# Kernel tuning notes

Hardware: AMD Instinct MI355X
Metric: run time of the kernel (lower is better)

The kernel has to match this reference:

```python
import jax, jax.numpy as jnp
import numpy as np

# module hyperparams (match init_kwargs)
C, K, S, RATIO, GC = 64, 7, 2, 2, 16
G = C // GC                      # 4 groups
KK = K * K                       # 49
NS = int(RATIO * S)              # 4
NN = NS * NS                     # 16
PAD = (K - 1) // 2               # 3
C1_IN = G * (2 * K * GC + KK)    # 1092
C1_OUT = G * NN * KK // 10       # 313
C2_OUT = G * NN * KK             # 3136
EPS = 1e-5


def _unfold(x, k, s, p):
    # torch.nn.Unfold: patches ordered (C, ki, kj) channel-major
    B, Cc, H, W = x.shape
    xp = jnp.pad(x, ((0, 0), (0, 0), (p, p), (p, p)))
    Ho = (H + 2 * p - k) // s + 1
    Wo = (W + 2 * p - k) // s + 1
    rows = jnp.arange(Ho)[:, None] * s + jnp.arange(k)[None, :]      # (Ho,k)
    cols = jnp.arange(Wo)[:, None] * s + jnp.arange(k)[None, :]      # (Wo,k)
    pat = xp[:, :, rows[:, :, None, None], cols[None, None, :, :]]   # (B,C,Ho,k,Wo,k)
    return pat.transpose(0, 1, 3, 5, 2, 4)                            # (B,C,k,k,Ho,Wo)


def setup_inputs() -> dict:
    key = jax.random.key(0)
    ks = jax.random.split(key, 5)
    x = jax.random.normal(ks[0], (8, C, 64, 64), dtype=jnp.float32)
    w1 = jax.random.normal(ks[1], (C1_OUT, C1_IN), dtype=jnp.float32) * 0.02
    gamma = jnp.ones((C1_OUT,), dtype=jnp.float32)   # BN weight (constant_init 1)
    beta = jnp.zeros((C1_OUT,), dtype=jnp.float32)   # BN bias
    w2 = jax.random.normal(ks[2], (C2_OUT, C1_OUT), dtype=jnp.float32) * 0.02
    b2 = jnp.zeros((C2_OUT,), dtype=jnp.float32)
    return {"x": x, "w1": w1, "gamma": gamma, "beta": beta, "w2": w2, "b2": b2}


def reference(x, w1, gamma, beta, w2, b2):
    B, _, H, W = x.shape
    pat = _unfold(x, K, S, PAD)                          # (B,C,K,K,Ho,Wo)
    Ho, Wo = pat.shape[-2], pat.shape[-1]
    xg = pat.reshape(B, G, GC, K, K, Ho, Wo)
    # three axis-wise max pools -> per-pixel descriptor
    x1 = xg.max(axis=2).reshape(B, G * K * K, Ho, Wo)
    x2 = xg.max(axis=3).reshape(B, G * GC * K, Ho, Wo)
    x3 = xg.max(axis=4).reshape(B, G * GC * K, Ho, Wo)
    feat = jnp.concatenate([x1, x2, x3], axis=1)         # (B, C1_IN, Ho, Wo)
    # conv1: 1x1 conv (no bias) + BN (batch stats) + ReLU
    h = jnp.einsum('bchw,oc->bohw', feat, w1)
    mu = h.mean(axis=(0, 2, 3), keepdims=True)
    var = h.var(axis=(0, 2, 3), keepdims=True)
    h = gamma[None, :, None, None] * (h - mu) * jax.lax.rsqrt(var + EPS) + beta[None, :, None, None]
    h = jax.nn.relu(h)
    # conv2: 1x1 conv with bias
    h2 = jnp.einsum('bchw,oc->bohw', h, w2) + b2[None, :, None, None]
    wt = h2.reshape(B, G, KK, NN, Ho, Wo)
    wt = jax.nn.softmax(wt, axis=2)                      # softmax over kernel positions
    # softmax-weighted patch reduction (mean over k*k)
    xk = xg.reshape(B, G, GC, KK, Ho, Wo)
    out = jnp.einsum('bgckhw,bgknhw->bgcnhw', xk, wt) / KK
    out = out.reshape(B, C, NS, NS, Ho, Wo)
    out = out.transpose(0, 1, 4, 2, 5, 3).reshape(B, C, Ho * NS, Wo * NS)
    return out
```

## Files before the change

kernel.cpp:

```cpp
#include <hip/hip_runtime.h>

namespace {
constexpr int kB    = 8;
constexpr int kC    = 64;
constexpr int kH    = 64, kW = 64;
constexpr int kNP   = 8192;
constexpr int kC1In = 1092;
constexpr int kKP   = 1152;
constexpr int kC1Out= 313;
constexpr int kC2Out= 3136;
constexpr int kC1P  = 320;
constexpr int kRowS = 56;
constexpr int kPosS = 16 * kRowS + 8;
}

typedef __attribute__((ext_vector_type(8))) short bf16x8;
typedef __attribute__((ext_vector_type(8))) _Float16 f16x8;
typedef __attribute__((ext_vector_type(2))) _Float16 h16x2;
typedef __attribute__((ext_vector_type(4))) float f32x4;

__device__ __forceinline__ unsigned short f2bf(float f) {
    unsigned u = __float_as_uint(f);
    unsigned r = (u + 0x7fffu + ((u >> 16) & 1u)) >> 16;
    return (unsigned short)r;
}

__global__ void k_w2split(const float* __restrict__ w2, bf16x8* __restrict__ w2t) {
    int idx = blockIdx.x * 256 + threadIdx.x;
    int lane = idx & 63;
    int t = (idx >> 6) % 10;
    int k = (idx / 640) % 49;
    int g = idx / 31360;
    int n = lane & 15, c0 = t * 32 + ((lane >> 4) << 3);
    int row = g * 784 + k * 16 + n;
    bf16x8 hi;
    #pragma unroll
    for (int e = 0; e < 8; ++e) {
        int c = c0 + e;
        float v = (c < kC1Out) ? w2[(size_t)row * kC1Out + c] : 0.f;
        hi[e] = (short)f2bf(v);
    }
    w2t[idx] = hi;
}

__global__ void k_w1cvt(const float* __restrict__ w1, unsigned short* __restrict__ w1s,
                        float* __restrict__ stats) {
    int idx = blockIdx.x * 256 + threadIdx.x;
    if (idx < 640) stats[idx] = 0.f;
    if (idx >= kC1P * kKP) return;
    int r = idx / kKP, c = idx - r * kKP;
    float v = (r < kC1Out && c < kC1In) ? w1[(size_t)r * kC1In + c] : 0.f;
    w1s[idx] = f2bf(v);
}

__global__ __launch_bounds__(256) void k_feat(const float* __restrict__ x,
                                              unsigned short* __restrict__ feat_bf) {
    __shared__ float xs[16 * 7 * 40];
    int tid = threadIdx.x;
    int g = blockIdx.x, pt = blockIdx.y;
    int p0 = pt * 16;
    int b = p0 >> 10, i = (p0 >> 5) & 31, j0 = p0 & 31;
    int y0 = 2 * i - 3, xbase = 2 * j0 - 3;
    const float* xb = x + ((size_t)(b * 64 + g * 16) << 12);

    for (int idx = tid; idx < 16 * 7 * 40; idx += 256) {
        int ch = idx / 280, r2 = idx - ch * 280;
        int row = r2 / 40, col = r2 - row * 40;
        int yy = y0 + row, xx = xbase + col;
        float v = 0.f;
        if ((unsigned)yy < 64u && (unsigned)xx < 64u)
            v = xb[(ch << 12) + (yy << 6) + xx];
        xs[idx] = v;
    }
    __syncthreads();

    for (int o = tid; o < 16 * 273; o += 256) {
        int pos = o / 273, c = o - pos * 273;
        float m = -INFINITY;
        int cg;
        if (c < 49) {
            int a = c / 7, bk = c - a * 7;
            int base = a * 40 + 2 * pos + bk;
            #pragma unroll
            for (int ch = 0; ch < 16; ++ch) m = fmaxf(m, xs[ch * 280 + base]);
            cg = g * 49 + c;
        } else if (c < 161) {
            int r = c - 49;
            int ch = r / 7, bk = r - ch * 7;
            int base = ch * 280 + 2 * pos + bk;
            #pragma unroll
            for (int a = 0; a < 7; ++a) m = fmaxf(m, xs[base + a * 40]);
            cg = 196 + g * 112 + r;
        } else {
            int r = c - 161;
            int ch = r / 7, a = r - ch * 7;
            int base = ch * 280 + a * 40 + 2 * pos;
            #pragma unroll
            for (int bk = 0; bk < 7; ++bk) m = fmaxf(m, xs[base + bk]);
            cg = 644 + g * 112 + r;
        }
        feat_bf[(size_t)(p0 + pos) * kKP + cg] = f2bf(m);
    }
    if (g == 3) {
        for (int idx = tid; idx < 16 * 60; idx += 256) {
            int pos = idx / 60, c = idx - pos * 60;
            feat_bf[(size_t)(p0 + pos) * kKP + 1092 + c] = 0;
        }
    }
}

__global__ __launch_bounds__(512) void k_gemm1(
        const unsigned short* __restrict__ feat_bf, const unsigned short* __restrict__ w1s,
        float* __restrict__ h, float* __restrict__ sum_, float* __restrict__ sumsq_) {
    __shared__ unsigned short Ald[128 * 64];
    __shared__ unsigned short Bld[64 * 64];
    __shared__ float lsum[64], lsq[64];
    int tid = threadIdx.x;
    int lane = tid & 63, wv = tid >> 6;
    int row0 = blockIdx.x * 128, col0 = blockIdx.y * 64;
    int wr = wv >> 1, wc = wv & 1;
    int srow = lane >> 3;
    int soct = (lane & 7) ^ srow;
    int frow = lane & 15, fk = lane >> 4;

    f32x4 acc[2][2] = {};
    for (int k0 = 0; k0 < kKP; k0 += 64) {
        #pragma unroll
        for (int qq = 0; qq < 3; ++qq) {
            int q = wv + qq * 8;
            const unsigned short* srcbase;
            unsigned short* dst;
            int grow;
            if (q < 16) { grow = row0 + q * 8 + srow; srcbase = feat_bf; dst = Ald + q * 512; }
            else        { grow = col0 + (q - 16) * 8 + srow; srcbase = w1s; dst = Bld + (q - 16) * 512; }
            const unsigned short* src = srcbase + (size_t)grow * kKP + k0 + soct * 8;
            __builtin_amdgcn_global_load_lds(
                (const __attribute__((address_space(1))) unsigned int*)src,
                (__attribute__((address_space(3))) unsigned int*)dst, 16, 0, 0);
        }
        __syncthreads();
        #pragma unroll
        for (int ks = 0; ks < 2; ++ks) {
            int oct = ks * 4 + fk;
            bf16x8 a0, a1, b0, b1;
            { int r = wr * 32 + frow;      a0 = *(const bf16x8*)(Ald + (r * 8 + (oct ^ (r & 7))) * 8); }
            { int r = wr * 32 + 16 + frow; a1 = *(const bf16x8*)(Ald + (r * 8 + (oct ^ (r & 7))) * 8); }
            { int r = wc * 32 + frow;      b0 = *(const bf16x8*)(Bld + (r * 8 + (oct ^ (r & 7))) * 8); }
            { int r = wc * 32 + 16 + frow; b1 = *(const bf16x8*)(Bld + (r * 8 + (oct ^ (r & 7))) * 8); }
            acc[0][0] = __builtin_amdgcn_mfma_f32_16x16x32_bf16(a0, b0, acc[0][0], 0, 0, 0);
            acc[0][1] = __builtin_amdgcn_mfma_f32_16x16x32_bf16(a0, b1, acc[0][1], 0, 0, 0);
            acc[1][0] = __builtin_amdgcn_mfma_f32_16x16x32_bf16(a1, b0, acc[1][0], 0, 0, 0);
            acc[1][1] = __builtin_amdgcn_mfma_f32_16x16x32_bf16(a1, b1, acc[1][1], 0, 0, 0);
        }
        __syncthreads();
    }

    if (tid < 64) { lsum[tid] = 0.f; lsq[tid] = 0.f; }
    __syncthreads();
    #pragma unroll
    for (int i = 0; i < 2; ++i) {
        int mrow = row0 + wr * 32 + i * 16 + (lane >> 4) * 4;
        #pragma unroll
        for (int j = 0; j < 2; ++j) {
            int col_l = wc * 32 + j * 16 + (lane & 15);
            float s = 0.f, sq = 0.f;
            #pragma unroll
            for (int r = 0; r < 4; ++r) {
                float v = acc[i][j][r];
                h[(size_t)(mrow + r) * kC1P + col0 + col_l] = v;
                s += v; sq += v * v;
            }
            atomicAdd(&lsum[col_l], s);
            atomicAdd(&lsq[col_l], sq);
        }
    }
    __syncthreads();
    if (tid < 64 && col0 + tid < kC1Out) {
        atomicAdd(&sum_[col0 + tid], lsum[tid]);
        atomicAdd(&sumsq_[col0 + tid], lsq[tid]);
    }
}

__global__ void k_finalize(const float* __restrict__ sum_, const float* __restrict__ sumsq_,
                           const float* __restrict__ gamma, const float* __restrict__ beta,
                           float* __restrict__ scale, float* __restrict__ shift) {
    int o = blockIdx.x * 256 + threadIdx.x;
    if (o >= kC1Out) return;
    float mu  = sum_[o]   * (1.f / kNP);
    float var = sumsq_[o] * (1.f / kNP) - mu * mu;
    float sc  = gamma[o] * rsqrtf(var + 1e-5f);
    scale[o] = sc;
    shift[o] = beta[o] - mu * sc;
}

__global__ void k_split_h(const float* __restrict__ h,
                          const float* __restrict__ scale, const float* __restrict__ shift,
                          bf16x8* __restrict__ ht_hi) {
    int idx = blockIdx.x * 256 + threadIdx.x;
    int lane = idx & 63;
    int t = (idx >> 6) % 10;
    int ptile = idx / 640;
    int pos = ptile * 16 + (lane & 15);
    int c0 = t * 32 + ((lane >> 4) << 3);
    float vv[8];
    *(float4*)&vv[0] = *(const float4*)(h + (size_t)pos * kC1P + c0);
    *(float4*)&vv[4] = *(const float4*)(h + (size_t)pos * kC1P + c0 + 4);
    bf16x8 hi;
    #pragma unroll
    for (int e = 0; e < 8; ++e) {
        int c = c0 + e;
        float v = (c < kC1Out) ? fmaxf(vv[e] * scale[c] + shift[c], 0.f) : 0.f;
        hi[e] = (short)f2bf(v);
    }
    ht_hi[idx] = hi;
}

__global__ __launch_bounds__(512) void k_fused(
        const bf16x8* __restrict__ ht_hi, const bf16x8* __restrict__ w2t,
        const float* __restrict__ b2, const float* __restrict__ x,
        float* __restrict__ out) {
    __shared__ _Float16 wtb[32 * kPosS];
    __shared__ float invt[512];
    int tid = threadIdx.x;
    int lane = tid & 63, wv = tid >> 6;
    int bid = blockIdx.x;
    int g = bid >> 8, pt = bid & 255;

    bf16x8 a0[10], a1[10];
    {
        const bf16x8* hb = ht_hi + (size_t)(pt * 2) * 640 + lane;
        #pragma unroll
        for (int t = 0; t < 10; ++t) { a0[t] = hb[t * 64]; a1[t] = hb[640 + t * 64]; }
    }

    int col = lane & 15, rgrp = lane >> 4;
    for (int k = wv; k < 49; k += 8) {
        f32x4 acc0 = {0.f, 0.f, 0.f, 0.f};
        f32x4 acc1 = {0.f, 0.f, 0.f, 0.f};
        const bf16x8* wb = w2t + ((size_t)(g * 49 + k) * 10) * 64 + lane;
        #pragma unroll
        for (int t = 0; t < 10; ++t) {
            bf16x8 bh = wb[t * 64];
            acc0 = __builtin_amdgcn_mfma_f32_16x16x32_bf16(a0[t], bh, acc0, 0, 0, 0);
            acc1 = __builtin_amdgcn_mfma_f32_16x16x32_bf16(a1[t], bh, acc1, 0, 0, 0);
        }
        float bias = b2[g * 784 + k * 16 + col];
        #pragma unroll
        for (int r = 0; r < 4; ++r) {
            int pos = rgrp * 4 + r;
            wtb[pos * kPosS + k * 16 + col]        = (_Float16)(acc0[r] + bias);
            wtb[(pos + 16) * kPosS + k * 16 + col] = (_Float16)(acc1[r] + bias);
        }
    }
    __syncthreads();

    {
        int pos = tid >> 4, n = tid & 15;
        const _Float16* baseA = wtb + pos * kPosS + n;
        f16x8 ee[7];
        float m = -INFINITY;
        #pragma unroll
        for (int c = 0; c < 7; ++c)
            #pragma unroll
            for (int e = 0; e < 8; ++e) {
                int k = c * 8 + e;
                if (k < 49) {
                    _Float16 v = baseA[k * 16];
                    ee[c][e] = v;
                    m = fmaxf(m, (float)v);
                } else ee[c][e] = (_Float16)0.f;
            }
        float s = 0.f;
        #pragma unroll
        for (int c = 0; c < 7; ++c)
            #pragma unroll
            for (int e = 0; e < 8; ++e) {
                int k = c * 8 + e;
                if (k < 49) {
                    float ex = __expf((float)ee[c][e] - m);
                    s += ex;
                    ee[c][e] = (_Float16)ex;
                }
            }
        __syncthreads();
        _Float16* baseB = wtb + pos * kPosS + n * kRowS;
        #pragma unroll
        for (int c = 0; c < 7; ++c) *(f16x8*)(baseB + c * 8) = ee[c];
        invt[tid] = 1.f / (s * 49.f);
    }
    __syncthreads();

    {
        int pos = tid & 31, c16 = tid >> 5;
        int p = pt * 32 + pos;
        int b = p >> 10, i = (p >> 5) & 31, j = p & 31;
        int y0 = 2 * i - 3, x0c = 2 * j - 3;
        const float* xc = x + (((size_t)b * 64 + g * 16 + c16) << 12);
        h16x2 patch2[28];
        #pragma unroll
        for (int a = 0; a < 7; ++a) {
            int yy = y0 + a;
            #pragma unroll
            for (int bk = 0; bk < 7; ++bk) {
                int kk = a * 7 + bk, xx = x0c + bk;
                float v = ((unsigned)yy < 64u && (unsigned)xx < 64u)
                        ? xc[(yy << 6) + xx] : 0.f;
                patch2[kk >> 1][kk & 1] = (_Float16)v;
            }
        }
        patch2[24][1] = (_Float16)0.f;
        patch2[25] = (h16x2)(_Float16)0.f;
        patch2[26] = (h16x2)(_Float16)0.f;
        patch2[27] = (h16x2)(_Float16)0.f;

        const _Float16* prow = wtb + pos * kPosS;
        float* outb = out + (((size_t)b * 64 + g * 16 + c16) << 14);
        #pragma unroll
        for (int n1 = 0; n1 < 4; ++n1) {
            f32x4 st;
            #pragma unroll
            for (int n2 = 0; n2 < 4; ++n2) {
                int n = n1 * 4 + n2;
                const f16x8* row = (const f16x8*)(prow + n * kRowS);
                float acc = 0.f;
                #pragma unroll
                for (int c = 0; c < 7; ++c) {
                    f16x8 w = row[c];
                    #pragma unroll
                    for (int q = 0; q < 4; ++q) {
                        h16x2 wp; wp[0] = w[2 * q]; wp[1] = w[2 * q + 1];
                        acc = __builtin_amdgcn_fdot2(patch2[c * 4 + q], wp, acc, false);
                    }
                }
                st[n2] = acc * invt[pos * 16 + n];
            }
            *(f32x4*)(outb + (i * 4 + n1) * 128 + j * 4) = st;
        }
    }
}

extern "C" void kernel_launch(void* const* d_in, const int* in_sizes, int n_in,
                              void* d_out, int out_size, void* d_ws, size_t ws_size,
                              hipStream_t stream) {
    const float* x     = (const float*)d_in[0];
    const float* w1    = (const float*)d_in[1];
    const float* gamma = (const float*)d_in[2];
    const float* beta  = (const float*)d_in[3];
    const float* w2    = (const float*)d_in[4];
    const float* b2    = (const float*)d_in[5];
    float* out = (float*)d_out;

    float* ws = (float*)d_ws;
    unsigned short* feat_bf = (unsigned short*)ws;
    float* h       = ws + 4718592;
    float* w2t_f   = h + 2621440;
    unsigned short* w1s = (unsigned short*)(w2t_f + 501760);
    float* sum_   = w2t_f + 501760 + 184320;
    float* sumsq_ = sum_ + 320;
    float* scale  = sumsq_ + 320;
    float* shift  = scale + 320;

    bf16x8* ht_hi = (bf16x8*)ws;
    bf16x8* w2t   = (bf16x8*)w2t_f;

    k_w2split<<<490, 256, 0, stream>>>(w2, w2t);
    k_w1cvt<<<(kC1P * kKP + 255) / 256, 256, 0, stream>>>(w1, w1s, sum_);
    k_feat<<<dim3(4, 512), 256, 0, stream>>>(x, feat_bf);
    k_gemm1<<<dim3(kNP / 128, 5), 512, 0, stream>>>(feat_bf, w1s, h, sum_, sumsq_);
    k_finalize<<<2, 256, 0, stream>>>(sum_, sumsq_, gamma, beta, scale, shift);
    k_split_h<<<1280, 256, 0, stream>>>(h, scale, shift, ht_hi);
    k_fused<<<1024, 512, 0, stream>>>(ht_hi, w2t, b2, x, out);
}
```

Baseline: 128.7 us.

## Merge preprocessing kernels, fold BN finalize into split, stage h tile in LDS

The three preprocessing kernels (feature pooling, w2 conversion, w1 conversion) become one launch that dispatches on block index. The BN finalize kernel is dropped and scale/shift are recomputed per element inside k_split_h. In k_fused, the A operand tile is now loaded into LDS via global_load_lds instead of being held in 20 bf16x8 registers per thread. Together these cut launch count and register pressure, at the cost of redundant BN math and extra LDS reads inside the MFMA loop.

```diff
diff --git a/kernel.cpp b/kernel.cpp
--- a/kernel.cpp
+++ b/kernel.cpp
@@ -12,6 +12,10 @@
 constexpr int kC1P  = 320;
 constexpr int kRowS = 56;
 constexpr int kPosS = 16 * kRowS + 8;
+constexpr int kPreFeat = 2048;
+constexpr int kPreW2   = 490;
+constexpr int kPreW1   = 1440;
+constexpr int kPreBlocks = kPreFeat + kPreW2 + kPreW1;
 }
 
 typedef __attribute__((ext_vector_type(8))) short bf16x8;
@@ -25,87 +29,87 @@
     return (unsigned short)r;
 }
 
-__global__ void k_w2split(const float* __restrict__ w2, bf16x8* __restrict__ w2t) {
-    int idx = blockIdx.x * 256 + threadIdx.x;
-    int lane = idx & 63;
-    int t = (idx >> 6) % 10;
-    int k = (idx / 640) % 49;
-    int g = idx / 31360;
-    int n = lane & 15, c0 = t * 32 + ((lane >> 4) << 3);
-    int row = g * 784 + k * 16 + n;
-    bf16x8 hi;
-    #pragma unroll
-    for (int e = 0; e < 8; ++e) {
-        int c = c0 + e;
-        float v = (c < kC1Out) ? w2[(size_t)row * kC1Out + c] : 0.f;
-        hi[e] = (short)f2bf(v);
-    }
-    w2t[idx] = hi;
-}
-
-__global__ void k_w1cvt(const float* __restrict__ w1, unsigned short* __restrict__ w1s,
-                        float* __restrict__ stats) {
-    int idx = blockIdx.x * 256 + threadIdx.x;
-    if (idx < 640) stats[idx] = 0.f;
-    if (idx >= kC1P * kKP) return;
-    int r = idx / kKP, c = idx - r * kKP;
-    float v = (r < kC1Out && c < kC1In) ? w1[(size_t)r * kC1In + c] : 0.f;
-    w1s[idx] = f2bf(v);
-}
-
-__global__ __launch_bounds__(256) void k_feat(const float* __restrict__ x,
-                                              unsigned short* __restrict__ feat_bf) {
+__global__ __launch_bounds__(256) void k_pre(const float* __restrict__ x,
+        const float* __restrict__ w1, const float* __restrict__ w2,
+        unsigned short* __restrict__ feat_bf, unsigned short* __restrict__ w1s,
+        bf16x8* __restrict__ w2t, float* __restrict__ stats) {
     __shared__ float xs[16 * 7 * 40];
     int tid = threadIdx.x;
-    int g = blockIdx.x, pt = blockIdx.y;
-    int p0 = pt * 16;
-    int b = p0 >> 10, i = (p0 >> 5) & 31, j0 = p0 & 31;
-    int y0 = 2 * i - 3, xbase = 2 * j0 - 3;
-    const float* xb = x + ((size_t)(b * 64 + g * 16) << 12);
-
-    for (int idx = tid; idx < 16 * 7 * 40; idx += 256) {
-        int ch = idx / 280, r2 = idx - ch * 280;
-        int row = r2 / 40, col = r2 - row * 40;
-        int yy = y0 + row, xx = xbase + col;
-        float v = 0.f;
-        if ((unsigned)yy < 64u && (unsigned)xx < 64u)
-            v = xb[(ch << 12) + (yy << 6) + xx];
-        xs[idx] = v;
-    }
-    __syncthreads();
-
-    for (int o = tid; o < 16 * 273; o += 256) {
-        int pos = o / 273, c = o - pos * 273;
-        float m = -INFINITY;
-        int cg;
-        if (c < 49) {
-            int a = c / 7, bk = c - a * 7;
-            int base = a * 40 + 2 * pos + bk;
-            #pragma unroll
-            for (int ch = 0; ch < 16; ++ch) m = fmaxf(m, xs[ch * 280 + base]);
-            cg = g * 49 + c;
-        } else if (c < 161) {
-            int r = c - 49;
-            int ch = r / 7, bk = r - ch * 7;
-            int base = ch * 280 + 2 * pos + bk;
-            #pragma unroll
-            for (int a = 0; a < 7; ++a) m = fmaxf(m, xs[base + a * 40]);
-            cg = 196 + g * 112 + r;
-        } else {
-            int r = c - 161;
-            int ch = r / 7, a = r - ch * 7;
-            int base = ch * 280 + a * 40 + 2 * pos;
-            #pragma unroll
-            for (int bk = 0; bk < 7; ++bk) m = fmaxf(m, xs[base + bk]);
-            cg = 644 + g * 112 + r;
-        }
-        feat_bf[(size_t)(p0 + pos) * kKP + cg] = f2bf(m);
-    }
-    if (g == 3) {
-        for (int idx = tid; idx < 16 * 60; idx += 256) {
-            int pos = idx / 60, c = idx - pos * 60;
-            feat_bf[(size_t)(p0 + pos) * kKP + 1092 + c] = 0;
-        }
+    int bid = blockIdx.x;
+
+    if (bid < kPreFeat) {
+        int g = bid >> 9, pt = bid & 511;
+        int p0 = pt * 16;
+        int b = p0 >> 10, i = (p0 >> 5) & 31, j0 = p0 & 31;
+        int y0 = 2 * i - 3, xbase = 2 * j0 - 3;
+        const float* xb = x + ((size_t)(b * 64 + g * 16) << 12);
+
+        for (int idx = tid; idx < 16 * 7 * 40; idx += 256) {
+            int ch = idx / 280, r2 = idx - ch * 280;
+            int row = r2 / 40, col = r2 - row * 40;
+            int yy = y0 + row, xx = xbase + col;
+            float v = 0.f;
+            if ((unsigned)yy < 64u && (unsigned)xx < 64u)
+                v = xb[(ch << 12) + (yy << 6) + xx];
+            xs[idx] = v;
+        }
+        __syncthreads();
+
+        for (int o = tid; o < 16 * 273; o += 256) {
+            int pos = o / 273, c = o - pos * 273;
+            float m = -INFINITY;
+            int cg;
+            if (c < 49) {
+                int a = c / 7, bk = c - a * 7;
+                int base = a * 40 + 2 * pos + bk;
+                #pragma unroll
+                for (int ch = 0; ch < 16; ++ch) m = fmaxf(m, xs[ch * 280 + base]);
+                cg = g * 49 + c;
+            } else if (c < 161) {
+                int r = c - 49;
+                int ch = r / 7, bk = r - ch * 7;
+                int base = ch * 280 + 2 * pos + bk;
+                #pragma unroll
+                for (int a = 0; a < 7; ++a) m = fmaxf(m, xs[base + a * 40]);
+                cg = 196 + g * 112 + r;
+            } else {
+                int r = c - 161;
+                int ch = r / 7, a = r - ch * 7;
+                int base = ch * 280 + a * 40 + 2 * pos;
+                #pragma unroll
+                for (int bk = 0; bk < 7; ++bk) m = fmaxf(m, xs[base + bk]);
+                cg = 644 + g * 112 + r;
+            }
+            feat_bf[(size_t)(p0 + pos) * kKP + cg] = f2bf(m);
+        }
+        if (g == 3) {
+            for (int idx = tid; idx < 16 * 60; idx += 256) {
+                int pos = idx / 60, c = idx - pos * 60;
+                feat_bf[(size_t)(p0 + pos) * kKP + 1092 + c] = 0;
+            }
+        }
+    } else if (bid < kPreFeat + kPreW2) {
+        int idx = (bid - kPreFeat) * 256 + tid;
+        int lane = idx & 63;
+        int t = (idx >> 6) % 10;
+        int k = (idx / 640) % 49;
+        int g = idx / 31360;
+        int n = lane & 15, c0 = t * 32 + ((lane >> 4) << 3);
+        int row = g * 784 + k * 16 + n;
+        bf16x8 hi;
+        #pragma unroll
+        for (int e = 0; e < 8; ++e) {
+            int c = c0 + e;
+            float v = (c < kC1Out) ? w2[(size_t)row * kC1Out + c] : 0.f;
+            hi[e] = (short)f2bf(v);
+        }
+        w2t[idx] = hi;
+    } else {
+        int idx = (bid - kPreFeat - kPreW2) * 256 + tid;
+        if (idx < 640) stats[idx] = 0.f;
+        int r = idx / kKP, c = idx - r * kKP;
+        float v = (r < kC1Out && c < kC1In) ? w1[(size_t)r * kC1In + c] : 0.f;
+        w1s[idx] = f2bf(v);
     }
 }
 
@@ -181,20 +185,9 @@
     }
 }
 
-__global__ void k_finalize(const float* __restrict__ sum_, const float* __restrict__ sumsq_,
-                           const float* __restrict__ gamma, const float* __restrict__ beta,
-                           float* __restrict__ scale, float* __restrict__ shift) {
-    int o = blockIdx.x * 256 + threadIdx.x;
-    if (o >= kC1Out) return;
-    float mu  = sum_[o]   * (1.f / kNP);
-    float var = sumsq_[o] * (1.f / kNP) - mu * mu;
-    float sc  = gamma[o] * rsqrtf(var + 1e-5f);
-    scale[o] = sc;
-    shift[o] = beta[o] - mu * sc;
-}
-
 __global__ void k_split_h(const float* __restrict__ h,
-                          const float* __restrict__ scale, const float* __restrict__ shift,
+                          const float* __restrict__ sum_, const float* __restrict__ sumsq_,
+                          const float* __restrict__ gamma, const float* __restrict__ beta,
                           bf16x8* __restrict__ ht_hi) {
     int idx = blockIdx.x * 256 + threadIdx.x;
     int lane = idx & 63;
@@ -209,7 +202,14 @@
     #pragma unroll
     for (int e = 0; e < 8; ++e) {
         int c = c0 + e;
-        float v = (c < kC1Out) ? fmaxf(vv[e] * scale[c] + shift[c], 0.f) : 0.f;
+        float v = 0.f;
+        if (c < kC1Out) {
+            float mu  = sum_[c]   * (1.f / kNP);
+            float var = sumsq_[c] * (1.f / kNP) - mu * mu;
+            float sc  = gamma[c] * rsqrtf(var + 1e-5f);
+            float sh  = beta[c] - mu * sc;
+            v = fmaxf(vv[e] * sc + sh, 0.f);
+        }
         hi[e] = (short)f2bf(v);
     }
     ht_hi[idx] = hi;
@@ -221,17 +221,24 @@
         float* __restrict__ out) {
     __shared__ _Float16 wtb[32 * kPosS];
     __shared__ float invt[512];
+    __shared__ bf16x8 htl[1280];
     int tid = threadIdx.x;
     int lane = tid & 63, wv = tid >> 6;
     int bid = blockIdx.x;
     int g = bid >> 8, pt = bid & 255;
 
-    bf16x8 a0[10], a1[10];
     {
-        const bf16x8* hb = ht_hi + (size_t)(pt * 2) * 640 + lane;
-        #pragma unroll
-        for (int t = 0; t < 10; ++t) { a0[t] = hb[t * 64]; a1[t] = hb[640 + t * 64]; }
-    }
+        const bf16x8* hb = ht_hi + (size_t)(pt * 2) * 640;
+        #pragma unroll
+        for (int r = 0; r < 3; ++r) {
+            int idx = r * 512 + tid;
+            if (idx < 1280)
+                __builtin_amdgcn_global_load_lds(
+                    (const __attribute__((address_space(1))) unsigned int*)(hb + idx),
+                    (__attribute__((address_space(3))) unsigned int*)(htl + idx), 16, 0, 0);
+        }
+    }
+    __syncthreads();
 
     int col = lane & 15, rgrp = lane >> 4;
     for (int k = wv; k < 49; k += 8) {
@@ -241,8 +248,10 @@
         #pragma unroll
         for (int t = 0; t < 10; ++t) {
             bf16x8 bh = wb[t * 64];
-            acc0 = __builtin_amdgcn_mfma_f32_16x16x32_bf16(a0[t], bh, acc0, 0, 0, 0);
-            acc1 = __builtin_amdgcn_mfma_f32_16x16x32_bf16(a1[t], bh, acc1, 0, 0, 0);
+            bf16x8 a0 = htl[t * 64 + lane];
+            bf16x8 a1 = htl[640 + t * 64 + lane];
+            acc0 = __builtin_amdgcn_mfma_f32_16x16x32_bf16(a0, bh, acc0, 0, 0, 0);
+            acc1 = __builtin_amdgcn_mfma_f32_16x16x32_bf16(a1, bh, acc1, 0, 0, 0);
         }
         float bias = b2[g * 784 + k * 16 + col];
         #pragma unroll
@@ -357,17 +366,12 @@
     unsigned short* w1s = (unsigned short*)(w2t_f + 501760);
     float* sum_   = w2t_f + 501760 + 184320;
     float* sumsq_ = sum_ + 320;
-    float* scale  = sumsq_ + 320;
-    float* shift  = scale + 320;
 
     bf16x8* ht_hi = (bf16x8*)ws;
     bf16x8* w2t   = (bf16x8*)w2t_f;
 
-    k_w2split<<<490, 256, 0, stream>>>(w2, w2t);
-    k_w1cvt<<<(kC1P * kKP + 255) / 256, 256, 0, stream>>>(w1, w1s, sum_);
-    k_feat<<<dim3(4, 512), 256, 0, stream>>>(x, feat_bf);
+    k_pre<<<kPreBlocks, 256, 0, stream>>>(x, w1, w2, feat_bf, w1s, w2t, sum_);
     k_gemm1<<<dim3(kNP / 128, 5), 512, 0, stream>>>(feat_bf, w1s, h, sum_, sumsq_);
-    k_finalize<<<2, 256, 0, stream>>>(sum_, sumsq_, gamma, beta, scale, shift);
-    k_split_h<<<1280, 256, 0, stream>>>(h, scale, shift, ht_hi);
+    k_split_h<<<1280, 256, 0, stream>>>(h, sum_, sumsq_, gamma, beta, ht_hi);
     k_fused<<<1024, 512, 0, stream>>>(ht_hi, w2t, b2, x, out);
 }
```

Measured after the change: 118.9 us. 1.08x faster.
